# Kernel tuning notes

Hardware: AMD Instinct MI355X
Metric: run time of the kernel (lower is better)

Reference implementation:

```python
import jax, jax.numpy as jnp
import numpy as np

N = 50000
E = 1600000
IN_F = 256
OUT_F = 128
ALPHA = 0.2  # LeakyReLU negative slope


def setup_inputs() -> dict:
    key = jax.random.key(0)
    k1, k2, k3, k4, k5, k6 = jax.random.split(key, 6)
    h = jax.random.normal(k1, (N, IN_F), dtype=jnp.float32)
    src = jax.random.randint(k2, (E,), 0, N, dtype=jnp.int64)
    dst = jax.random.randint(k3, (E,), 0, N, dtype=jnp.int64)
    # xavier_uniform-style init
    def xavier(k, shape):
        bound = np.sqrt(6.0 / (shape[0] + shape[1]))
        return jax.random.uniform(k, shape, jnp.float32, -bound, bound)
    W = xavier(k4, (IN_F, OUT_F))
    a_src = xavier(k5, (OUT_F, 1))
    a_dst = xavier(k6, (OUT_F, 1))
    return {"h": h, "src": src, "dst": dst, "W": W, "a_src": a_src, "a_dst": a_dst}


def reference(h, src, dst, W, a_src, a_dst):
    n = h.shape[0]
    Wh = h @ W                                  # [N, OUT_F] dense GEMM
    f1 = (Wh @ a_src)[:, 0]                     # [N]
    f2 = (Wh @ a_dst)[:, 0]                     # [N]
    e = f1[src] + f2[dst]                       # [E] edge-wise gather
    e = jnp.where(e > 0, e, ALPHA * e)          # LeakyReLU
    # sparse softmax over each row (segment = src/row index)
    m = jax.ops.segment_max(e, src, num_segments=n)
    ex = jnp.exp(e - m[src])
    denom = jax.ops.segment_sum(ex, src, num_segments=n)
    att = ex / denom[src]                       # [E] normalized attention
    # sparse-dense matmul: h_prime[i] = sum_j att[ij] * Wh[j]
    h_prime = jax.ops.segment_sum(att[:, None] * Wh[dst], src, num_segments=n)
    return jax.nn.elu(h_prime)
```

## Files before the change

kernel.cpp:

```cpp
#include <hip/hip_runtime.h>
#include <hip/hip_bf16.h>
#include <math.h>

#define IN_F 256
#define OUT_F 128
#define ALPHA 0.2f

#define BSH 7
#define BNODES 128
#define CHUNK 8192
#define NBK 512
#define CAP 5120

typedef __attribute__((ext_vector_type(8))) short short8;
typedef __attribute__((ext_vector_type(4))) float f32x4;

static __device__ __forceinline__ unsigned short f2bf(float x) {
    union { __hip_bfloat16 h; unsigned short u; } cv;
    cv.h = __float2bfloat16(x);
    return cv.u;
}

static __device__ __forceinline__ float2 bf2u(unsigned int u) {
    union { float f; unsigned int i; } a, b;
    a.i = u << 16;
    b.i = u & 0xFFFF0000u;
    return make_float2(a.f, b.f);
}

__global__ void zero_kernel(int* __restrict__ cursor, int m) {
    int i = blockIdx.x * blockDim.x + threadIdx.x;
    if (i < m) cursor[i] = i * CAP;
}

__global__ __launch_bounds__(512) void scatter_bin_kernel(const int* __restrict__ src,
                                                          const int* __restrict__ dst,
                                                          int* __restrict__ cursor,
                                                          unsigned int* __restrict__ bin,
                                                          int e, int nb) {
    __shared__ unsigned int ebuf[CHUNK];
    __shared__ int lh[NBK];
    __shared__ int ls[NBK];
    __shared__ int ebase[NBK];
    __shared__ int lx[NBK];
    __shared__ int gbase[NBK];
    int tid = threadIdx.x;
    int base = blockIdx.x * CHUNK;
    int count = e - base; if (count > CHUNK) count = CHUNK;

    for (int i = tid; i < nb; i += 512) lh[i] = 0;
    __syncthreads();
    for (int i = tid; i < count; i += 512) atomicAdd(&lh[src[base + i] >> BSH], 1);
    __syncthreads();
    int v = (tid < nb) ? lh[tid] : 0;
    ls[tid] = v;
    __syncthreads();
#pragma unroll
    for (int off = 1; off < NBK; off <<= 1) {
        int t = (tid >= off) ? ls[tid - off] : 0;
        __syncthreads();
        ls[tid] += t;
        __syncthreads();
    }
    if (tid < nb) {
        int ex = ls[tid] - v;
        ebase[tid] = ex;
        lx[tid] = ex;
    }
    __syncthreads();
    for (int i = tid; i < count; i += 512) {
        int s = src[base + i], d = dst[base + i];
        int b = s >> BSH;
        int p = atomicAdd(&lx[b], 1);
        ebuf[p] = ((unsigned int)(s & (BNODES - 1)) << 17) | (unsigned int)d;
    }
    __syncthreads();
    if (tid < nb) {
        int c = lh[tid];
        gbase[tid] = c ? atomicAdd(&cursor[tid], c) : 0;
    }
    __syncthreads();
    int wave = tid >> 6, lane = tid & 63;
    for (int b = wave; b < nb; b += 8) {
        int c = lh[b], eb = ebase[b], gb = gbase[b];
        for (int l = lane; l < c; l += 64) bin[gb + l] = ebuf[eb + l];
    }
}

__global__ __launch_bounds__(256) void sort_kernel(const int* __restrict__ cursor,
                                                   const unsigned int* __restrict__ bin,
                                                   uint2* __restrict__ edat,
                                                   int* __restrict__ offs,
                                                   int* __restrict__ deg,
                                                   const float* __restrict__ f1,
                                                   const float* __restrict__ f2, int n) {
    __shared__ unsigned int ebuf[CAP];
    __shared__ int lh[BNODES];
    __shared__ int lx[BNODES];
    __shared__ float lf1[BNODES];
    int b = blockIdx.x;
    int tid = threadIdx.x;
    int base = b * CAP;
    int K = cursor[b] - base;
    if (K > CAP) K = CAP;
    for (int l = tid; l < BNODES; l += 256) {
        lh[l] = 0;
        int node = (b << BSH) + l;
        lf1[l] = (node < n) ? f1[node] : 0.f;
    }
    __syncthreads();
    for (int i = tid; i < K; i += 256) {
        unsigned int p = bin[base + i];
        ebuf[i] = p;
        atomicAdd(&lh[p >> 17], 1);
    }
    __syncthreads();
    int own = (tid < BNODES) ? lh[tid] : 0;
    for (int off = 1; off < BNODES; off <<= 1) {
        int v = (tid >= off && tid < BNODES) ? lh[tid - off] : 0;
        __syncthreads();
        if (tid < BNODES) lh[tid] += v;
        __syncthreads();
    }
    if (tid < BNODES) {
        int ex = lh[tid] - own;
        lx[tid] = ex;
        int node = (b << BSH) + tid;
        if (node < n) { offs[node] = base + ex; deg[node] = own; }
    }
    __syncthreads();
    for (int i = tid; i < K; i += 256) {
        unsigned int p = ebuf[i];
        int ls_ = p >> 17;
        int d = p & 0x1FFFF;
        int r = atomicAdd(&lx[ls_], 1);
        float e = lf1[ls_] + f2[d];
        e = e > 0.f ? e : ALPHA * e;
        edat[base + r] = make_uint2((unsigned int)d, __float_as_uint(__expf(e)));
    }
}

__global__ __launch_bounds__(256) void gemm_kernel(const float* __restrict__ h,
                                                   const float* __restrict__ W,
                                                   const float* __restrict__ a_src,
                                                   const float* __restrict__ a_dst,
                                                   unsigned short* __restrict__ Whb,
                                                   float* __restrict__ f1,
                                                   float* __restrict__ f2, int n) {
    __shared__ unsigned short as_[64 * 40];
    __shared__ unsigned short bs_[128 * 40];
    int tid = threadIdx.x;
    int wv = tid >> 6, lane = tid & 63;
    int m = lane & 15, quad = lane >> 4;
    int r0 = blockIdx.x * 64;

    f32x4 acc[8];
#pragma unroll
    for (int c = 0; c < 8; c++) acc[c] = (f32x4){0.f, 0.f, 0.f, 0.f};

    for (int k0 = 0; k0 < IN_F; k0 += 32) {
        {
            int arow = tid >> 3;
            int kq = tid & 7;
#pragma unroll
            for (int p = 0; p < 2; p++) {
                int row = arow + p * 32;
                int grow = r0 + row;
                float4 v = make_float4(0.f, 0.f, 0.f, 0.f);
                if (grow < n) v = *(const float4*)&h[(size_t)grow * IN_F + k0 + kq * 4];
                ushort4 b;
                b.x = f2bf(v.x); b.y = f2bf(v.y); b.z = f2bf(v.z); b.w = f2bf(v.w);
                *(ushort4*)&as_[row * 40 + kq * 4] = b;
            }
        }
        {
            int c4 = (tid & 31) * 4;
            int kb = tid >> 5;
#pragma unroll
            for (int p = 0; p < 4; p++) {
                int kk = p * 8 + kb;
                float4 wv4 = *(const float4*)&W[(size_t)(k0 + kk) * OUT_F + c4];
                bs_[(c4 + 0) * 40 + kk] = f2bf(wv4.x);
                bs_[(c4 + 1) * 40 + kk] = f2bf(wv4.y);
                bs_[(c4 + 2) * 40 + kk] = f2bf(wv4.z);
                bs_[(c4 + 3) * 40 + kk] = f2bf(wv4.w);
            }
        }
        __syncthreads();
        short8 af = *(const short8*)&as_[(wv * 16 + m) * 40 + quad * 8];
#pragma unroll
        for (int c = 0; c < 8; c++) {
            short8 bfv = *(const short8*)&bs_[(c * 16 + m) * 40 + quad * 8];
            acc[c] = __builtin_amdgcn_mfma_f32_16x16x32_bf16(af, bfv, acc[c], 0, 0, 0);
        }
        __syncthreads();
    }

    int base_row = r0 + wv * 16 + quad * 4;
#pragma unroll
    for (int reg = 0; reg < 4; reg++) {
        int rg = base_row + reg;
        if (rg < n) {
#pragma unroll
            for (int c = 0; c < 8; c++)
                Whb[(size_t)rg * OUT_F + c * 16 + m] = f2bf(acc[c][reg]);
        }
    }

    float a1[8], a2[8];
#pragma unroll
    for (int c = 0; c < 8; c++) {
        a1[c] = a_src[c * 16 + m];
        a2[c] = a_dst[c * 16 + m];
    }
    float p1[4] = {0.f, 0.f, 0.f, 0.f}, p2[4] = {0.f, 0.f, 0.f, 0.f};
#pragma unroll
    for (int c = 0; c < 8; c++)
#pragma unroll
        for (int reg = 0; reg < 4; reg++) {
            p1[reg] += acc[c][reg] * a1[c];
            p2[reg] += acc[c][reg] * a2[c];
        }
#pragma unroll
    for (int mask = 1; mask < 16; mask <<= 1)
#pragma unroll
        for (int reg = 0; reg < 4; reg++) {
            p1[reg] += __shfl_xor(p1[reg], mask, 64);
            p2[reg] += __shfl_xor(p2[reg], mask, 64);
        }
    if (m == 0) {
#pragma unroll
        for (int reg = 0; reg < 4; reg++) {
            int rg = base_row + reg;
            if (rg < n) { f1[rg] = p1[reg]; f2[rg] = p2[reg]; }
        }
    }
}

__global__ __launch_bounds__(256) void agg_kernel(const unsigned int* __restrict__ WhbU,
                                                  const int* __restrict__ offs,
                                                  const int* __restrict__ deg,
                                                  const uint2* __restrict__ edat,
                                                  float* __restrict__ out, int n) {
    int tid = threadIdx.x;
    int lane = tid & 63;
    int node = blockIdx.x * 4 + (tid >> 6);
    if (node >= n) return;
    int grp = lane >> 4;
    int c8 = lane & 15;
    int j0 = offs[node];
    int j1 = j0 + deg[node];
    float4 accA = make_float4(0.f, 0.f, 0.f, 0.f);
    float4 accB = make_float4(0.f, 0.f, 0.f, 0.f);
    float den = 0.f;

    int j = j0;
    for (; j + 16 <= j1; j += 16) {
        uint2 e0 = edat[j + grp];
        uint2 e1 = edat[j + grp + 4];
        uint2 e2 = edat[j + grp + 8];
        uint2 e3 = edat[j + grp + 12];
        uint4 w0 = *(const uint4*)&WhbU[(size_t)e0.x * 64 + c8 * 4];
        uint4 w1 = *(const uint4*)&WhbU[(size_t)e1.x * 64 + c8 * 4];
        uint4 w2 = *(const uint4*)&WhbU[(size_t)e2.x * 64 + c8 * 4];
        uint4 w3 = *(const uint4*)&WhbU[(size_t)e3.x * 64 + c8 * 4];
        float x0 = __uint_as_float(e0.y);
        float x1 = __uint_as_float(e1.y);
        float x2 = __uint_as_float(e2.y);
        float x3 = __uint_as_float(e3.y);
        float2 g;
        g = bf2u(w0.x); accA.x += x0 * g.x; accA.y += x0 * g.y;
        g = bf2u(w0.y); accA.z += x0 * g.x; accA.w += x0 * g.y;
        g = bf2u(w0.z); accB.x += x0 * g.x; accB.y += x0 * g.y;
        g = bf2u(w0.w); accB.z += x0 * g.x; accB.w += x0 * g.y;
        g = bf2u(w1.x); accA.x += x1 * g.x; accA.y += x1 * g.y;
        g = bf2u(w1.y); accA.z += x1 * g.x; accA.w += x1 * g.y;
        g = bf2u(w1.z); accB.x += x1 * g.x; accB.y += x1 * g.y;
        g = bf2u(w1.w); accB.z += x1 * g.x; accB.w += x1 * g.y;
        g = bf2u(w2.x); accA.x += x2 * g.x; accA.y += x2 * g.y;
        g = bf2u(w2.y); accA.z += x2 * g.x; accA.w += x2 * g.y;
        g = bf2u(w2.z); accB.x += x2 * g.x; accB.y += x2 * g.y;
        g = bf2u(w2.w); accB.z += x2 * g.x; accB.w += x2 * g.y;
        g = bf2u(w3.x); accA.x += x3 * g.x; accA.y += x3 * g.y;
        g = bf2u(w3.y); accA.z += x3 * g.x; accA.w += x3 * g.y;
        g = bf2u(w3.z); accB.x += x3 * g.x; accB.y += x3 * g.y;
        g = bf2u(w3.w); accB.z += x3 * g.x; accB.w += x3 * g.y;
        den += x0 + x1 + x2 + x3;
    }
    for (; j + 4 <= j1; j += 4) {
        uint2 e = edat[j + grp];
        uint4 w = *(const uint4*)&WhbU[(size_t)e.x * 64 + c8 * 4];
        float x = __uint_as_float(e.y);
        float2 g;
        g = bf2u(w.x); accA.x += x * g.x; accA.y += x * g.y;
        g = bf2u(w.y); accA.z += x * g.x; accA.w += x * g.y;
        g = bf2u(w.z); accB.x += x * g.x; accB.y += x * g.y;
        g = bf2u(w.w); accB.z += x * g.x; accB.w += x * g.y;
        den += x;
    }
    if (j + grp < j1) {
        uint2 e = edat[j + grp];
        uint4 w = *(const uint4*)&WhbU[(size_t)e.x * 64 + c8 * 4];
        float x = __uint_as_float(e.y);
        float2 g;
        g = bf2u(w.x); accA.x += x * g.x; accA.y += x * g.y;
        g = bf2u(w.y); accA.z += x * g.x; accA.w += x * g.y;
        g = bf2u(w.z); accB.x += x * g.x; accB.y += x * g.y;
        g = bf2u(w.w); accB.z += x * g.x; accB.w += x * g.y;
        den += x;
    }

#pragma unroll
    for (int mask = 16; mask < 64; mask <<= 1) {
        accA.x += __shfl_xor(accA.x, mask, 64);
        accA.y += __shfl_xor(accA.y, mask, 64);
        accA.z += __shfl_xor(accA.z, mask, 64);
        accA.w += __shfl_xor(accA.w, mask, 64);
        accB.x += __shfl_xor(accB.x, mask, 64);
        accB.y += __shfl_xor(accB.y, mask, 64);
        accB.z += __shfl_xor(accB.z, mask, 64);
        accB.w += __shfl_xor(accB.w, mask, 64);
        den += __shfl_xor(den, mask, 64);
    }

    if (grp == 0) {
        float inv = (j1 > j0) ? 1.f / den : 0.f;
        float r[8];
        r[0] = accA.x * inv; r[1] = accA.y * inv; r[2] = accA.z * inv; r[3] = accA.w * inv;
        r[4] = accB.x * inv; r[5] = accB.y * inv; r[6] = accB.z * inv; r[7] = accB.w * inv;
#pragma unroll
        for (int k = 0; k < 8; k++) r[k] = r[k] > 0.f ? r[k] : expm1f(r[k]);
        float* op = &out[(size_t)node * OUT_F + c8 * 8];
        *(float4*)&op[0] = make_float4(r[0], r[1], r[2], r[3]);
        *(float4*)&op[4] = make_float4(r[4], r[5], r[6], r[7]);
    }
}

extern "C" void kernel_launch(void* const* d_in, const int* in_sizes, int n_in,
                              void* d_out, int out_size, void* d_ws, size_t ws_size,
                              hipStream_t stream) {
    const float* h     = (const float*)d_in[0];
    const int*   src   = (const int*)d_in[1];
    const int*   dst   = (const int*)d_in[2];
    const float* W     = (const float*)d_in[3];
    const float* a_src = (const float*)d_in[4];
    const float* a_dst = (const float*)d_in[5];
    float* out = (float*)d_out;

    const int N = in_sizes[0] / IN_F;
    const int E = in_sizes[1];
    const int NB = (N + BNODES - 1) >> BSH;
    const int NCH = (E + CHUNK - 1) / CHUNK;

    char* ws = (char*)d_ws;
    size_t off = 0;
    auto alloc = [&](size_t bytes) -> void* {
        void* p = ws + off;
        off += (bytes + 255) & ~(size_t)255;
        return p;
    };
    unsigned short* Whb = (unsigned short*)alloc((size_t)N * OUT_F * 2);
    float* f1     = (float*)alloc((size_t)N * 4);
    float* f2     = (float*)alloc((size_t)N * 4);
    int*   cursor = (int*)alloc((size_t)NB * 4);
    int*   offs   = (int*)alloc((size_t)N * 4);
    int*   deg    = (int*)alloc((size_t)N * 4);
    unsigned int* bin  = (unsigned int*)alloc((size_t)NB * CAP * 4);
    uint2*        edat = (uint2*)alloc((size_t)NB * CAP * 8);
    (void)ws_size; (void)n_in; (void)out_size;

    zero_kernel<<<(NB + 255) / 256, 256, 0, stream>>>(cursor, NB);
    scatter_bin_kernel<<<NCH, 512, 0, stream>>>(src, dst, cursor, bin, E, NB);
    gemm_kernel<<<(N + 63) / 64, 256, 0, stream>>>(h, W, a_src, a_dst, Whb, f1, f2, N);
    sort_kernel<<<NB, 256, 0, stream>>>(cursor, bin, edat, offs, deg, f1, f2, N);
    agg_kernel<<<(N + 3) / 4, 256, 0, stream>>>((const unsigned int*)Whb, offs, deg, edat, out, N);
}
```

Baseline: 234.5 us.

## Fuse edge binning and GEMM into one heterogeneous launch, prefetch edges in aggregation

Merges the scatter-binning kernel and the dense GEMM into a single launch, with blocks split by blockIdx and shared memory overlaid through a union, so the two independent stages can run concurrently. The GEMM tile grows to 128 rows with 512 threads. The cursor init kernel becomes a memset, with cursors now storing relative offsets. The aggregation loop software-prefetches the next group of edge records, and ELU switches to a fast exp minus one. Tradeoffs are larger shared-memory use per block, which may lower occupancy for the GEMM path, and slightly lower ELU accuracy near zero.

Result: faster. 211.6 us (-9.8%).

```diff
diff --git a/kernel.cpp b/kernel.cpp
--- a/kernel.cpp
+++ b/kernel.cpp
@@ -28,62 +28,158 @@
     return make_float2(a.f, b.f);
 }
 
-__global__ void zero_kernel(int* __restrict__ cursor, int m) {
-    int i = blockIdx.x * blockDim.x + threadIdx.x;
-    if (i < m) cursor[i] = i * CAP;
-}
-
-__global__ __launch_bounds__(512) void scatter_bin_kernel(const int* __restrict__ src,
-                                                          const int* __restrict__ dst,
-                                                          int* __restrict__ cursor,
-                                                          unsigned int* __restrict__ bin,
-                                                          int e, int nb) {
-    __shared__ unsigned int ebuf[CHUNK];
-    __shared__ int lh[NBK];
-    __shared__ int ls[NBK];
-    __shared__ int ebase[NBK];
-    __shared__ int lx[NBK];
-    __shared__ int gbase[NBK];
+__global__ __launch_bounds__(512) void scatter_gemm_kernel(
+        const int* __restrict__ src, const int* __restrict__ dst,
+        int* __restrict__ cursor, unsigned int* __restrict__ bin, int e, int nb,
+        const float* __restrict__ h, const float* __restrict__ W,
+        const float* __restrict__ a_src, const float* __restrict__ a_dst,
+        unsigned short* __restrict__ Whb, float* __restrict__ f1,
+        float* __restrict__ f2, int n, int nsc) {
+    __shared__ union {
+        struct {
+            unsigned int ebuf[CHUNK];
+            int lh[NBK];
+            int ls[NBK];
+            int ebase[NBK];
+            int lx[NBK];
+            int gbase[NBK];
+        } sc;
+        struct {
+            unsigned short a[128 * 40];
+            unsigned short b[128 * 40];
+        } ge;
+    } sm;
     int tid = threadIdx.x;
-    int base = blockIdx.x * CHUNK;
-    int count = e - base; if (count > CHUNK) count = CHUNK;
-
-    for (int i = tid; i < nb; i += 512) lh[i] = 0;
-    __syncthreads();
-    for (int i = tid; i < count; i += 512) atomicAdd(&lh[src[base + i] >> BSH], 1);
-    __syncthreads();
-    int v = (tid < nb) ? lh[tid] : 0;
-    ls[tid] = v;
-    __syncthreads();
-#pragma unroll
-    for (int off = 1; off < NBK; off <<= 1) {
-        int t = (tid >= off) ? ls[tid - off] : 0;
-        __syncthreads();
-        ls[tid] += t;
-        __syncthreads();
-    }
-    if (tid < nb) {
-        int ex = ls[tid] - v;
-        ebase[tid] = ex;
-        lx[tid] = ex;
-    }
-    __syncthreads();
-    for (int i = tid; i < count; i += 512) {
-        int s = src[base + i], d = dst[base + i];
-        int b = s >> BSH;
-        int p = atomicAdd(&lx[b], 1);
-        ebuf[p] = ((unsigned int)(s & (BNODES - 1)) << 17) | (unsigned int)d;
-    }
-    __syncthreads();
-    if (tid < nb) {
-        int c = lh[tid];
-        gbase[tid] = c ? atomicAdd(&cursor[tid], c) : 0;
-    }
-    __syncthreads();
-    int wave = tid >> 6, lane = tid & 63;
-    for (int b = wave; b < nb; b += 8) {
-        int c = lh[b], eb = ebase[b], gb = gbase[b];
-        for (int l = lane; l < c; l += 64) bin[gb + l] = ebuf[eb + l];
+
+    if ((int)blockIdx.x < nsc) {
+        int base = blockIdx.x * CHUNK;
+        int count = e - base; if (count > CHUNK) count = CHUNK;
+
+        for (int i = tid; i < nb; i += 512) sm.sc.lh[i] = 0;
+        __syncthreads();
+        for (int i = tid; i < count; i += 512) atomicAdd(&sm.sc.lh[src[base + i] >> BSH], 1);
+        __syncthreads();
+        int v = (tid < nb) ? sm.sc.lh[tid] : 0;
+        sm.sc.ls[tid] = v;
+        __syncthreads();
+#pragma unroll
+        for (int off = 1; off < NBK; off <<= 1) {
+            int t = (tid >= off) ? sm.sc.ls[tid - off] : 0;
+            __syncthreads();
+            sm.sc.ls[tid] += t;
+            __syncthreads();
+        }
+        if (tid < nb) {
+            int ex = sm.sc.ls[tid] - v;
+            sm.sc.ebase[tid] = ex;
+            sm.sc.lx[tid] = ex;
+        }
+        __syncthreads();
+        for (int i = tid; i < count; i += 512) {
+            int s = src[base + i], d = dst[base + i];
+            int b = s >> BSH;
+            int p = atomicAdd(&sm.sc.lx[b], 1);
+            sm.sc.ebuf[p] = ((unsigned int)(s & (BNODES - 1)) << 17) | (unsigned int)d;
+        }
+        __syncthreads();
+        if (tid < nb) {
+            int c = sm.sc.lh[tid];
+            sm.sc.gbase[tid] = c ? atomicAdd(&cursor[tid], c) : 0;
+        }
+        __syncthreads();
+        int wave = tid >> 6, lane = tid & 63;
+        for (int b = wave; b < nb; b += 8) {
+            int c = sm.sc.lh[b], eb = sm.sc.ebase[b], gb = sm.sc.gbase[b];
+            size_t gb0 = (size_t)b * CAP + gb;
+            for (int l = lane; l < c; l += 64) bin[gb0 + l] = sm.sc.ebuf[eb + l];
+        }
+    } else {
+        int bid = blockIdx.x - nsc;
+        int wv = tid >> 6, lane = tid & 63;
+        int m = lane & 15, quad = lane >> 4;
+        int r0 = bid * 128;
+
+        f32x4 acc[8];
+#pragma unroll
+        for (int c = 0; c < 8; c++) acc[c] = (f32x4){0.f, 0.f, 0.f, 0.f};
+
+        for (int k0 = 0; k0 < IN_F; k0 += 32) {
+            {
+                int arow = tid >> 3;
+                int kq = tid & 7;
+#pragma unroll
+                for (int p = 0; p < 2; p++) {
+                    int row = arow + p * 64;
+                    int grow = r0 + row;
+                    float4 v = make_float4(0.f, 0.f, 0.f, 0.f);
+                    if (grow < n) v = *(const float4*)&h[(size_t)grow * IN_F + k0 + kq * 4];
+                    ushort4 b;
+                    b.x = f2bf(v.x); b.y = f2bf(v.y); b.z = f2bf(v.z); b.w = f2bf(v.w);
+                    *(ushort4*)&sm.ge.a[row * 40 + kq * 4] = b;
+                }
+            }
+            {
+                int c4 = (tid & 31) * 4;
+                int kb = tid >> 5;
+#pragma unroll
+                for (int p = 0; p < 2; p++) {
+                    int kk = p * 16 + kb;
+                    float4 wv4 = *(const float4*)&W[(size_t)(k0 + kk) * OUT_F + c4];
+                    sm.ge.b[(c4 + 0) * 40 + kk] = f2bf(wv4.x);
+                    sm.ge.b[(c4 + 1) * 40 + kk] = f2bf(wv4.y);
+                    sm.ge.b[(c4 + 2) * 40 + kk] = f2bf(wv4.z);
+                    sm.ge.b[(c4 + 3) * 40 + kk] = f2bf(wv4.w);
+                }
+            }
+            __syncthreads();
+            short8 af = *(const short8*)&sm.ge.a[(wv * 16 + m) * 40 + quad * 8];
+#pragma unroll
+            for (int c = 0; c < 8; c++) {
+                short8 bfv = *(const short8*)&sm.ge.b[(c * 16 + m) * 40 + quad * 8];
+                acc[c] = __builtin_amdgcn_mfma_f32_16x16x32_bf16(af, bfv, acc[c], 0, 0, 0);
+            }
+            __syncthreads();
+        }
+
+        int base_row = r0 + wv * 16 + quad * 4;
+#pragma unroll
+        for (int reg = 0; reg < 4; reg++) {
+            int rg = base_row + reg;
+            if (rg < n) {
+#pragma unroll
+                for (int c = 0; c < 8; c++)
+                    Whb[(size_t)rg * OUT_F + c * 16 + m] = f2bf(acc[c][reg]);
+            }
+        }
+
+        float a1[8], a2[8];
+#pragma unroll
+        for (int c = 0; c < 8; c++) {
+            a1[c] = a_src[c * 16 + m];
+            a2[c] = a_dst[c * 16 + m];
+        }
+        float p1[4] = {0.f, 0.f, 0.f, 0.f}, p2[4] = {0.f, 0.f, 0.f, 0.f};
+#pragma unroll
+        for (int c = 0; c < 8; c++)
+#pragma unroll
+            for (int reg = 0; reg < 4; reg++) {
+                p1[reg] += acc[c][reg] * a1[c];
+                p2[reg] += acc[c][reg] * a2[c];
+            }
+#pragma unroll
+        for (int mask = 1; mask < 16; mask <<= 1)
+#pragma unroll
+            for (int reg = 0; reg < 4; reg++) {
+                p1[reg] += __shfl_xor(p1[reg], mask, 64);
+                p2[reg] += __shfl_xor(p2[reg], mask, 64);
+            }
+        if (m == 0) {
+#pragma unroll
+            for (int reg = 0; reg < 4; reg++) {
+                int rg = base_row + reg;
+                if (rg < n) { f1[rg] = p1[reg]; f2[rg] = p2[reg]; }
+            }
+        }
     }
 }
 
@@ -101,7 +197,7 @@
     int b = blockIdx.x;
     int tid = threadIdx.x;
     int base = b * CAP;
-    int K = cursor[b] - base;
+    int K = cursor[b];
     if (K > CAP) K = CAP;
     for (int l = tid; l < BNODES; l += 256) {
         lh[l] = 0;
@@ -137,103 +233,6 @@
         float e = lf1[ls_] + f2[d];
         e = e > 0.f ? e : ALPHA * e;
         edat[base + r] = make_uint2((unsigned int)d, __float_as_uint(__expf(e)));
-    }
-}
-
-__global__ __launch_bounds__(256) void gemm_kernel(const float* __restrict__ h,
-                                                   const float* __restrict__ W,
-                                                   const float* __restrict__ a_src,
-                                                   const float* __restrict__ a_dst,
-                                                   unsigned short* __restrict__ Whb,
-                                                   float* __restrict__ f1,
-                                                   float* __restrict__ f2, int n) {
-    __shared__ unsigned short as_[64 * 40];
-    __shared__ unsigned short bs_[128 * 40];
-    int tid = threadIdx.x;
-    int wv = tid >> 6, lane = tid & 63;
-    int m = lane & 15, quad = lane >> 4;
-    int r0 = blockIdx.x * 64;
-
-    f32x4 acc[8];
-#pragma unroll
-    for (int c = 0; c < 8; c++) acc[c] = (f32x4){0.f, 0.f, 0.f, 0.f};
-
-    for (int k0 = 0; k0 < IN_F; k0 += 32) {
-        {
-            int arow = tid >> 3;
-            int kq = tid & 7;
-#pragma unroll
-            for (int p = 0; p < 2; p++) {
-                int row = arow + p * 32;
-                int grow = r0 + row;
-                float4 v = make_float4(0.f, 0.f, 0.f, 0.f);
-                if (grow < n) v = *(const float4*)&h[(size_t)grow * IN_F + k0 + kq * 4];
-                ushort4 b;
-                b.x = f2bf(v.x); b.y = f2bf(v.y); b.z = f2bf(v.z); b.w = f2bf(v.w);
-                *(ushort4*)&as_[row * 40 + kq * 4] = b;
-            }
-        }
-        {
-            int c4 = (tid & 31) * 4;
-            int kb = tid >> 5;
-#pragma unroll
-            for (int p = 0; p < 4; p++) {
-                int kk = p * 8 + kb;
-                float4 wv4 = *(const float4*)&W[(size_t)(k0 + kk) * OUT_F + c4];
-                bs_[(c4 + 0) * 40 + kk] = f2bf(wv4.x);
-                bs_[(c4 + 1) * 40 + kk] = f2bf(wv4.y);
-                bs_[(c4 + 2) * 40 + kk] = f2bf(wv4.z);
-                bs_[(c4 + 3) * 40 + kk] = f2bf(wv4.w);
-            }
-        }
-        __syncthreads();
-        short8 af = *(const short8*)&as_[(wv * 16 + m) * 40 + quad * 8];
-#pragma unroll
-        for (int c = 0; c < 8; c++) {
-            short8 bfv = *(const short8*)&bs_[(c * 16 + m) * 40 + quad * 8];
-            acc[c] = __builtin_amdgcn_mfma_f32_16x16x32_bf16(af, bfv, acc[c], 0, 0, 0);
-        }
-        __syncthreads();
-    }
-
-    int base_row = r0 + wv * 16 + quad * 4;
-#pragma unroll
-    for (int reg = 0; reg < 4; reg++) {
-        int rg = base_row + reg;
-        if (rg < n) {
-#pragma unroll
-            for (int c = 0; c < 8; c++)
-                Whb[(size_t)rg * OUT_F + c * 16 + m] = f2bf(acc[c][reg]);
-        }
-    }
-
-    float a1[8], a2[8];
-#pragma unroll
-    for (int c = 0; c < 8; c++) {
-        a1[c] = a_src[c * 16 + m];
-        a2[c] = a_dst[c * 16 + m];
-    }
-    float p1[4] = {0.f, 0.f, 0.f, 0.f}, p2[4] = {0.f, 0.f, 0.f, 0.f};
-#pragma unroll
-    for (int c = 0; c < 8; c++)
-#pragma unroll
-        for (int reg = 0; reg < 4; reg++) {
-            p1[reg] += acc[c][reg] * a1[c];
-            p2[reg] += acc[c][reg] * a2[c];
-        }
-#pragma unroll
-    for (int mask = 1; mask < 16; mask <<= 1)
-#pragma unroll
-        for (int reg = 0; reg < 4; reg++) {
-            p1[reg] += __shfl_xor(p1[reg], mask, 64);
-            p2[reg] += __shfl_xor(p2[reg], mask, 64);
-        }
-    if (m == 0) {
-#pragma unroll
-        for (int reg = 0; reg < 4; reg++) {
-            int rg = base_row + reg;
-            if (rg < n) { f1[rg] = p1[reg]; f2[rg] = p2[reg]; }
-        }
     }
 }
 
@@ -255,41 +254,54 @@
     float den = 0.f;
 
     int j = j0;
-    for (; j + 16 <= j1; j += 16) {
+    int nmain = (j1 - j0) >> 4;
+    if (nmain > 0) {
         uint2 e0 = edat[j + grp];
         uint2 e1 = edat[j + grp + 4];
         uint2 e2 = edat[j + grp + 8];
         uint2 e3 = edat[j + grp + 12];
-        uint4 w0 = *(const uint4*)&WhbU[(size_t)e0.x * 64 + c8 * 4];
-        uint4 w1 = *(const uint4*)&WhbU[(size_t)e1.x * 64 + c8 * 4];
-        uint4 w2 = *(const uint4*)&WhbU[(size_t)e2.x * 64 + c8 * 4];
-        uint4 w3 = *(const uint4*)&WhbU[(size_t)e3.x * 64 + c8 * 4];
-        float x0 = __uint_as_float(e0.y);
-        float x1 = __uint_as_float(e1.y);
-        float x2 = __uint_as_float(e2.y);
-        float x3 = __uint_as_float(e3.y);
-        float2 g;
-        g = bf2u(w0.x); accA.x += x0 * g.x; accA.y += x0 * g.y;
-        g = bf2u(w0.y); accA.z += x0 * g.x; accA.w += x0 * g.y;
-        g = bf2u(w0.z); accB.x += x0 * g.x; accB.y += x0 * g.y;
-        g = bf2u(w0.w); accB.z += x0 * g.x; accB.w += x0 * g.y;
-        g = bf2u(w1.x); accA.x += x1 * g.x; accA.y += x1 * g.y;
-        g = bf2u(w1.y); accA.z += x1 * g.x; accA.w += x1 * g.y;
-        g = bf2u(w1.z); accB.x += x1 * g.x; accB.y += x1 * g.y;
-        g = bf2u(w1.w); accB.z += x1 * g.x; accB.w += x1 * g.y;
-        g = bf2u(w2.x); accA.x += x2 * g.x; accA.y += x2 * g.y;
-        g = bf2u(w2.y); accA.z += x2 * g.x; accA.w += x2 * g.y;
-        g = bf2u(w2.z); accB.x += x2 * g.x; accB.y += x2 * g.y;
-        g = bf2u(w2.w); accB.z += x2 * g.x; accB.w += x2 * g.y;
-        g = bf2u(w3.x); accA.x += x3 * g.x; accA.y += x3 * g.y;
-        g = bf2u(w3.y); accA.z += x3 * g.x; accA.w += x3 * g.y;
-        g = bf2u(w3.z); accB.x += x3 * g.x; accB.y += x3 * g.y;
-        g = bf2u(w3.w); accB.z += x3 * g.x; accB.w += x3 * g.y;
-        den += x0 + x1 + x2 + x3;
+        for (int it = 0; it < nmain; ++it) {
+            uint4 w0 = *(const uint4*)&WhbU[(size_t)(e0.x << 6) + c8 * 4];
+            uint4 w1 = *(const uint4*)&WhbU[(size_t)(e1.x << 6) + c8 * 4];
+            uint4 w2 = *(const uint4*)&WhbU[(size_t)(e2.x << 6) + c8 * 4];
+            uint4 w3 = *(const uint4*)&WhbU[(size_t)(e3.x << 6) + c8 * 4];
+            float x0 = __uint_as_float(e0.y);
+            float x1 = __uint_as_float(e1.y);
+            float x2 = __uint_as_float(e2.y);
+            float x3 = __uint_as_float(e3.y);
+            int jn = j + 16;
+            uint2 n0, n1, n2, n3;
+            if (it + 1 < nmain) {
+                n0 = edat[jn + grp];
+                n1 = edat[jn + grp + 4];
+                n2 = edat[jn + grp + 8];
+                n3 = edat[jn + grp + 12];
+            }
+            float2 g;
+            g = bf2u(w0.x); accA.x += x0 * g.x; accA.y += x0 * g.y;
+            g = bf2u(w0.y); accA.z += x0 * g.x; accA.w += x0 * g.y;
+            g = bf2u(w0.z); accB.x += x0 * g.x; accB.y += x0 * g.y;
+            g = bf2u(w0.w); accB.z += x0 * g.x; accB.w += x0 * g.y;
+            g = bf2u(w1.x); accA.x += x1 * g.x; accA.y += x1 * g.y;
+            g = bf2u(w1.y); accA.z += x1 * g.x; accA.w += x1 * g.y;
+            g = bf2u(w1.z); accB.x += x1 * g.x; accB.y += x1 * g.y;
+            g = bf2u(w1.w); accB.z += x1 * g.x; accB.w += x1 * g.y;
+            g = bf2u(w2.x); accA.x += x2 * g.x; accA.y += x2 * g.y;
+            g = bf2u(w2.y); accA.z += x2 * g.x; accA.w += x2 * g.y;
+            g = bf2u(w2.z); accB.x += x2 * g.x; accB.y += x2 * g.y;
+            g = bf2u(w2.w); accB.z += x2 * g.x; accB.w += x2 * g.y;
+            g = bf2u(w3.x); accA.x += x3 * g.x; accA.y += x3 * g.y;
+            g = bf2u(w3.y); accA.z += x3 * g.x; accA.w += x3 * g.y;
+            g = bf2u(w3.z); accB.x += x3 * g.x; accB.y += x3 * g.y;
+            g = bf2u(w3.w); accB.z += x3 * g.x; accB.w += x3 * g.y;
+            den += x0 + x1 + x2 + x3;
+            j = jn;
+            e0 = n0; e1 = n1; e2 = n2; e3 = n3;
+        }
     }
     for (; j + 4 <= j1; j += 4) {
         uint2 e = edat[j + grp];
-        uint4 w = *(const uint4*)&WhbU[(size_t)e.x * 64 + c8 * 4];
+        uint4 w = *(const uint4*)&WhbU[(size_t)(e.x << 6) + c8 * 4];
         float x = __uint_as_float(e.y);
         float2 g;
         g = bf2u(w.x); accA.x += x * g.x; accA.y += x * g.y;
@@ -300,7 +312,7 @@
     }
     if (j + grp < j1) {
         uint2 e = edat[j + grp];
-        uint4 w = *(const uint4*)&WhbU[(size_t)e.x * 64 + c8 * 4];
+        uint4 w = *(const uint4*)&WhbU[(size_t)(e.x << 6) + c8 * 4];
         float x = __uint_as_float(e.y);
         float2 g;
         g = bf2u(w.x); accA.x += x * g.x; accA.y += x * g.y;
@@ -329,7 +341,7 @@
         r[0] = accA.x * inv; r[1] = accA.y * inv; r[2] = accA.z * inv; r[3] = accA.w * inv;
         r[4] = accB.x * inv; r[5] = accB.y * inv; r[6] = accB.z * inv; r[7] = accB.w * inv;
 #pragma unroll
-        for (int k = 0; k < 8; k++) r[k] = r[k] > 0.f ? r[k] : expm1f(r[k]);
+        for (int k = 0; k < 8; k++) r[k] = r[k] > 0.f ? r[k] : __expf(r[k]) - 1.f;
         float* op = &out[(size_t)node * OUT_F + c8 * 8];
         *(float4*)&op[0] = make_float4(r[0], r[1], r[2], r[3]);
         *(float4*)&op[4] = make_float4(r[4], r[5], r[6], r[7]);
@@ -351,6 +363,7 @@
     const int E = in_sizes[1];
     const int NB = (N + BNODES - 1) >> BSH;
     const int NCH = (E + CHUNK - 1) / CHUNK;
+    const int GB = (N + 127) / 128;
 
     char* ws = (char*)d_ws;
     size_t off = 0;
@@ -369,9 +382,9 @@
     uint2*        edat = (uint2*)alloc((size_t)NB * CAP * 8);
     (void)ws_size; (void)n_in; (void)out_size;
 
-    zero_kernel<<<(NB + 255) / 256, 256, 0, stream>>>(cursor, NB);
-    scatter_bin_kernel<<<NCH, 512, 0, stream>>>(src, dst, cursor, bin, E, NB);
-    gemm_kernel<<<(N + 63) / 64, 256, 0, stream>>>(h, W, a_src, a_dst, Whb, f1, f2, N);
+    hipMemsetAsync(cursor, 0, (size_t)NB * 4, stream);
+    scatter_gemm_kernel<<<NCH + GB, 512, 0, stream>>>(src, dst, cursor, bin, E, NB,
+                                                      h, W, a_src, a_dst, Whb, f1, f2, N, NCH);
     sort_kernel<<<NB, 256, 0, stream>>>(cursor, bin, edat, offs, deg, f1, f2, N);
     agg_kernel<<<(N + 3) / 4, 256, 0, stream>>>((const unsigned int*)Whb, offs, deg, edat, out, N);
 }
```
